# Kernel optimization log

Measured on AMD Instinct MI355X. Metric: run time of the kernel, lower is better.

## Reference

```python
import jax, jax.numpy as jnp
import numpy as np

N, L, C, H, W, HEAD = 16, 256, 512, 32, 32, 16

def setup_inputs() -> dict:
    key = jax.random.key(0)
    ks = jax.random.split(key, 8)
    s = 0.02  # weight init scale
    return {
        "feature": jax.random.normal(ks[0], (N, C, H, W), jnp.float32),
        "token": jax.random.normal(ks[1], (N, L, C), jnp.float32),
        "wq": jax.random.normal(ks[2], (C, C), jnp.float32) * s,
        "bq": jax.random.normal(ks[3], (C,), jnp.float32) * s,
        "wk": jax.random.normal(ks[4], (C, C), jnp.float32) * s,
        "bk": jax.random.normal(ks[5], (C,), jnp.float32) * s,
        "wv": jax.random.normal(ks[6], (C, C), jnp.float32) * s,
        "bv": jax.random.normal(ks[7], (C,), jnp.float32) * s,
    }

def reference(feature, token, wq, bq, wk, bk, wv, bv):
    n, c, hgt, wid = feature.shape
    h = HEAD
    d = c // h
    l = token.shape[1]
    scale = jnp.asarray(np.sqrt(c / h), feature.dtype)
    tok = token.transpose(0, 2, 1)  # (N, C, L)
    # 1x1 conv projections == per-position GEMMs
    v = (jnp.einsum('ncl,dc->ndl', tok, wv) + bv[None, :, None]).reshape(n, h, d, l)
    k = (jnp.einsum('ncl,dc->ndl', tok, wk) + bk[None, :, None]).reshape(n, h, d, l)
    q = (jnp.einsum('nchw,dc->ndhw', feature, wq) + bq[None, :, None, None])
    q = q.reshape(n, h, d, hgt * wid).transpose(0, 1, 3, 2)  # (N, h, HW, d)
    scores = jnp.einsum('nhqd,nhdl->nhql', q, k) / scale  # (N, h, HW, L)
    coef = jax.nn.softmax(scores, axis=-1)
    proj = jnp.einsum('nhdl,nhql->nhdq', v, coef)  # (N, h, d, HW)
    return feature + proj.reshape(n, c, hgt, wid)
```

## Files before the change

kernel.cpp:

```cpp
#include <hip/hip_runtime.h>
#include <hip/hip_bf16.h>

#define N_ 16
#define L_ 256
#define C_ 512
#define HW_ 1024
#define HEADS_ 16
#define DH_ 32

typedef unsigned short u16;
typedef unsigned int u32;
typedef __attribute__((ext_vector_type(8))) short short8_t;
typedef __attribute__((ext_vector_type(4))) float f32x4;

__device__ __forceinline__ u16 f2bs(float f) {
    union { float f; u32 i; } x; x.f = f;
    u32 r = x.i + 0x7fffu + ((x.i >> 16) & 1u);
    return (u16)(r >> 16);
}
__device__ __forceinline__ u32 cvt_pk_bf16(float lo, float hi) {
    u32 r;
    asm("v_cvt_pk_bf16_f32 %0, %1, %2" : "=v"(r) : "v"(lo), "v"(hi));
    return r;
}
__device__ __forceinline__ void cvt8(const float* __restrict__ src, void* dst) {
    float4 lo = *(const float4*)src;
    float4 hi = *(const float4*)(src + 4);
    union { u32 w[4]; short8_t v; } pk;
    pk.w[0] = cvt_pk_bf16(lo.x, lo.y);
    pk.w[1] = cvt_pk_bf16(lo.z, lo.w);
    pk.w[2] = cvt_pk_bf16(hi.x, hi.y);
    pk.w[3] = cvt_pk_bf16(hi.z, hi.w);
    *(short8_t*)dst = pk.v;
}
#define AS1(p) (const __attribute__((address_space(1))) void*)(p)
#define AS3(p) (__attribute__((address_space(3))) void*)(p)

__global__ __launch_bounds__(256) void prep_kv_kernel(
    const float* __restrict__ feature, const float* __restrict__ token,
    const float* __restrict__ wq, const float* __restrict__ wk,
    const float* __restrict__ wv, const float* __restrict__ bk,
    const float* __restrict__ bv,
    u16* __restrict__ Ftb, u16* __restrict__ wqb,
    u16* __restrict__ Kout, u16* __restrict__ Vt)
{
    __shared__ __align__(16) unsigned char smem[32768];
    const int t = threadIdx.x;

    if (blockIdx.x < 2048) {
        float (*LT)[67] = (float(*)[67])smem;
        const int tidx = blockIdx.x;
        const int pb = tidx & 15, cb = (tidx >> 4) & 7, n = tidx >> 7;
        const int c0 = cb * 64, pos0 = pb * 64;

        #pragma unroll
        for (int r = 0; r < 4; ++r) {
            const int c = r * 16 + (t >> 4);
            const int p = (t & 15) * 4;
            float4 v = *(const float4*)&feature[
                ((size_t)n * C_ + c0 + c) * HW_ + pos0 + p];
            LT[c][p] = v.x; LT[c][p+1] = v.y; LT[c][p+2] = v.z; LT[c][p+3] = v.w;
        }
        __syncthreads();
        #pragma unroll
        for (int rep = 0; rep < 2; ++rep) {
            const int pos = (t >> 3) + rep * 32;
            const int c = (t & 7) * 8;
            u16 tmp[8];
            #pragma unroll
            for (int j = 0; j < 8; ++j) tmp[j] = f2bs(LT[c + j][pos]);
            *(short8_t*)&Ftb[(size_t)(n * HW_ + pos0 + pos) * C_ + c0 + c] =
                *(short8_t*)tmp;
        }
    } else if (blockIdx.x < 2304) {
        const int kvid = blockIdx.x - 2048;
        const int xcd = kvid & 7, j = kvid >> 3;
        const int m0 = (xcd * 4 + (j & 3)) * 128;
        const int n0 = (j >> 2) * 64;
        const int lane = t & 63, wid = t >> 6;
        const int i16 = lane & 15, g = lane >> 4;
        const int wm = wid >> 1, wn = wid & 1;
        const int r8 = t >> 3, c8 = t & 7;
        u16* Tok = (u16*)smem;
        u16* Bk  = (u16*)(smem + 16384);
        u16* Bv  = (u16*)(smem + 24576);
        u16 (*LTo)[72] = (u16(*)[72])smem;

        f32x4 ak[4][2], av[4][2];
        #pragma unroll
        for (int mt = 0; mt < 4; ++mt)
            #pragma unroll
            for (int nt = 0; nt < 2; ++nt) {
                ak[mt][nt] = (f32x4){0.f, 0.f, 0.f, 0.f};
                av[mt][nt] = (f32x4){0.f, 0.f, 0.f, 0.f};
            }

        for (int c0 = 0; c0 < C_; c0 += 64) {
            __syncthreads();
            #pragma unroll
            for (int p = 0; p < 4; ++p) {
                const int m = p * 32 + r8;
                cvt8(&token[(size_t)(m0 + m) * C_ + c0 + c8 * 8],
                     &Tok[m * 64 + ((c8 ^ (m & 7)) << 3)]);
            }
            #pragma unroll
            for (int p = 0; p < 2; ++p) {
                const int m = p * 32 + r8;
                const int sw = m * 64 + ((c8 ^ (m & 7)) << 3);
                cvt8(&wk[(size_t)(n0 + m) * C_ + c0 + c8 * 8], &Bk[sw]);
                cvt8(&wv[(size_t)(n0 + m) * C_ + c0 + c8 * 8], &Bv[sw]);
            }
            __syncthreads();
            #pragma unroll
            for (int ks = 0; ks < 2; ++ks) {
                short8_t a[4], bbk[2], bbv[2];
                #pragma unroll
                for (int mt = 0; mt < 4; ++mt) {
                    const int m = wm * 64 + mt * 16 + i16;
                    a[mt] = *(const short8_t*)&Tok[m * 64 + ((((ks << 2) | g) ^ (m & 7)) << 3)];
                }
                #pragma unroll
                for (int nt = 0; nt < 2; ++nt) {
                    const int d = wn * 32 + nt * 16 + i16;
                    const int sw = d * 64 + ((((ks << 2) | g) ^ (d & 7)) << 3);
                    bbk[nt] = *(const short8_t*)&Bk[sw];
                    bbv[nt] = *(const short8_t*)&Bv[sw];
                }
                #pragma unroll
                for (int mt = 0; mt < 4; ++mt)
                    #pragma unroll
                    for (int nt = 0; nt < 2; ++nt) {
                        ak[mt][nt] = __builtin_amdgcn_mfma_f32_16x16x32_bf16(
                            a[mt], bbk[nt], ak[mt][nt], 0, 0, 0);
                        av[mt][nt] = __builtin_amdgcn_mfma_f32_16x16x32_bf16(
                            a[mt], bbv[nt], av[mt][nt], 0, 0, 0);
                    }
            }
        }
        const int nb = m0 >> 8, l0 = m0 & 255;
        const size_t vtbase = (size_t)nb * C_ * L_;
        #pragma unroll
        for (int nt = 0; nt < 2; ++nt) {
            const int d = n0 + wn * 32 + nt * 16 + i16;
            const float bb = bv[d];
            #pragma unroll
            for (int mt = 0; mt < 4; ++mt) {
                ushort4 w;
                w.x = f2bs(av[mt][nt][0] + bb);
                w.y = f2bs(av[mt][nt][1] + bb);
                w.z = f2bs(av[mt][nt][2] + bb);
                w.w = f2bs(av[mt][nt][3] + bb);
                const int l = l0 + wm * 64 + mt * 16 + g * 4;
                *(ushort4*)&Vt[vtbase + (size_t)d * L_ + l] = w;
            }
        }
        __syncthreads();
        #pragma unroll
        for (int nt = 0; nt < 2; ++nt) {
            const int col = wn * 32 + nt * 16 + i16;
            const float bb = bk[n0 + col];
            #pragma unroll
            for (int mt = 0; mt < 4; ++mt)
                #pragma unroll
                for (int r = 0; r < 4; ++r)
                    LTo[wm * 64 + mt * 16 + g * 4 + r][col] = f2bs(ak[mt][nt][r] + bb);
        }
        __syncthreads();
        #pragma unroll
        for (int rep = 0; rep < 4; ++rep) {
            const int m = (t >> 3) + rep * 32;
            const int cs2 = (t & 7) * 8;
            *(short8_t*)&Kout[(size_t)(m0 + m) * C_ + n0 + cs2] = *(short8_t*)&LTo[m][cs2];
        }
    } else {
        const int idx = (blockIdx.x - 2304) * 256 + t;
        float4 v = ((const float4*)wq)[idx];
        ushort4 w;
        w.x = f2bs(v.x); w.y = f2bs(v.y); w.z = f2bs(v.z); w.w = f2bs(v.w);
        ((ushort4*)wqb)[idx] = w;
    }
}

__global__ __launch_bounds__(256) void gemm_q_kernel(
    const u16* __restrict__ Ftb, const u16* __restrict__ wqb,
    const float* __restrict__ bq, u16* __restrict__ Qout)
{
    __shared__ __align__(16) unsigned char smem[65536];

    const int t = threadIdx.x;
    const int lane = t & 63, wid = t >> 6;
    const int i16 = lane & 15, g = lane >> 4;
    const int r8 = t >> 3, gr = t & 7;

    const int qid = blockIdx.x;
    const int xcd = qid & 7, loc = qid >> 3;
    const int m0 = (xcd * 16 + (loc & 15)) * 128;
    const int n0 = (loc >> 4) * 128;
    const int wm = wid >> 1, wn = wid & 1;
    u16 (*LTo)[136] = (u16(*)[136])smem;

    f32x4 aq[4][4];
    #pragma unroll
    for (int mt = 0; mt < 4; ++mt)
        #pragma unroll
        for (int nt = 0; nt < 4; ++nt)
            aq[mt][nt] = (f32x4){0.f, 0.f, 0.f, 0.f};

    #define Q_STAGE(buf, c0) { \
        _Pragma("unroll") \
        for (int p = 0; p < 4; ++p) { \
            const int row = p * 32 + r8; \
            const int gs = (gr ^ (row & 7)) << 3; \
            __builtin_amdgcn_global_load_lds( \
                AS1(Ftb + (size_t)(m0 + row) * C_ + (c0) + gs), \
                AS3(smem + (buf) * 32768 + (p * 32 + wid * 8) * 128), 16, 0, 0); \
            __builtin_amdgcn_global_load_lds( \
                AS1(wqb + (size_t)(n0 + row) * C_ + (c0) + gs), \
                AS3(smem + (buf) * 32768 + 16384 + (p * 32 + wid * 8) * 128), 16, 0, 0); } }

    Q_STAGE(0, 0);
    __syncthreads();
    #pragma unroll
    for (int cs = 0; cs < 8; ++cs) {
        const int cur = cs & 1;
        if (cs < 7) Q_STAGE(cur ^ 1, (cs + 1) * 64);
        const u16* Ft = (const u16*)(smem + cur * 32768);
        const u16* Bq = (const u16*)(smem + cur * 32768 + 16384);
        #pragma unroll
        for (int ks = 0; ks < 2; ++ks) {
            short8_t a[4], b[4];
            #pragma unroll
            for (int mt = 0; mt < 4; ++mt) {
                const int m = wm * 64 + mt * 16 + i16;
                a[mt] = *(const short8_t*)&Ft[m * 64 + ((((ks << 2) | g) ^ (m & 7)) << 3)];
            }
            #pragma unroll
            for (int nt = 0; nt < 4; ++nt) {
                const int d = wn * 64 + nt * 16 + i16;
                b[nt] = *(const short8_t*)&Bq[d * 64 + ((((ks << 2) | g) ^ (d & 7)) << 3)];
            }
            #pragma unroll
            for (int mt = 0; mt < 4; ++mt)
                #pragma unroll
                for (int nt = 0; nt < 4; ++nt)
                    aq[mt][nt] = __builtin_amdgcn_mfma_f32_16x16x32_bf16(
                        a[mt], b[nt], aq[mt][nt], 0, 0, 0);
        }
        __syncthreads();
    }
    #pragma unroll
    for (int half = 0; half < 2; ++half) {
        __syncthreads();
        if (wm == half) {
            #pragma unroll
            for (int nt = 0; nt < 4; ++nt) {
                const int col = wn * 64 + nt * 16 + i16;
                const float bb = bq[n0 + col];
                #pragma unroll
                for (int mt = 0; mt < 4; ++mt)
                    #pragma unroll
                    for (int r = 0; r < 4; ++r)
                        LTo[mt * 16 + g * 4 + r][col] = f2bs(aq[mt][nt][r] + bb);
            }
        }
        __syncthreads();
        #pragma unroll
        for (int rep = 0; rep < 4; ++rep) {
            const int row = rep * 16 + (t >> 4);
            const int col = (t & 15) * 8;
            *(short8_t*)&Qout[(size_t)(m0 + half * 64 + row) * C_ + n0 + col] =
                *(short8_t*)&LTo[row][col];
        }
    }
}

__global__ __launch_bounds__(256) void attn_kernel(
    const u16* __restrict__ Qws, const u16* __restrict__ Kws,
    const u16* __restrict__ Vws, const float* __restrict__ feature,
    float* __restrict__ out)
{
    __shared__ __align__(16) unsigned char smem[32768];

    const int t = threadIdx.x;
    const int wid = t >> 6, lane = t & 63;
    const int i16 = lane & 15, g = lane >> 4;
    const int pt = blockIdx.x, h = blockIdx.y, n = blockIdx.z;
    const int pos0 = pt * 64;
    const size_t qbase = ((size_t)n * HW_ + pos0) * C_ + h * DH_;
    const size_t kbase = ((size_t)n * L_) * C_ + h * DH_;
    const size_t vbase = (size_t)n * C_ * L_ + (size_t)h * DH_ * L_;

    const int q = wid * 16 + i16;

    short8_t bq = *(const short8_t*)&Qws[qbase + (size_t)q * C_ + g * 8];

    #pragma unroll
    for (int p = 0; p < 4; ++p) {
        const int kg = (lane & 3) ^ ((lane >> 3) & 3);
        const int kr = wid * 64 + p * 16 + (lane >> 2);
        const u16* ksrc = Kws + kbase + (size_t)kr * C_ + kg * 8;
        __builtin_amdgcn_global_load_lds(AS1(ksrc),
            AS3(smem + wid * 4096 + p * 1024), 16, 0, 0);
        const int vd = wid * 8 + p * 2 + (lane >> 5);
        const u16* vsrc = Vws + vbase + (size_t)vd * L_ + ((lane & 31) ^ (vd & 7)) * 8;
        __builtin_amdgcn_global_load_lds(AS1(vsrc),
            AS3(smem + 16384 + wid * 4096 + p * 1024), 16, 0, 0);
    }
    __syncthreads();

    const int kgr = g ^ ((i16 >> 1) & 3);
    f32x4 s[16];
    #pragma unroll
    for (int nf = 0; nf < 16; ++nf) {
        short8_t a = *(const short8_t*)(smem + (nf * 16 + i16) * 64 + kgr * 16);
        f32x4 z = {0.f, 0.f, 0.f, 0.f};
        s[nf] = __builtin_amdgcn_mfma_f32_16x16x32_bf16(a, bq, z, 0, 0, 0);
    }

    float mm[16], sm[16];
    #pragma unroll
    for (int nf = 0; nf < 16; ++nf)
        mm[nf] = fmaxf(fmaxf(s[nf][0], s[nf][1]), fmaxf(s[nf][2], s[nf][3]));
    #pragma unroll
    for (int st = 8; st >= 1; st >>= 1)
        #pragma unroll
        for (int i = 0; i < 8; ++i)
            if (i < st) mm[i] = fmaxf(mm[i], mm[i + st]);
    float m = mm[0];
    m = fmaxf(m, __shfl_xor(m, 16));
    m = fmaxf(m, __shfl_xor(m, 32));

    const float K2 = 0.25506288f;
    #pragma unroll
    for (int nf = 0; nf < 16; ++nf) {
        #pragma unroll
        for (int r = 0; r < 4; ++r) s[nf][r] = exp2f((s[nf][r] - m) * K2);
        sm[nf] = (s[nf][0] + s[nf][1]) + (s[nf][2] + s[nf][3]);
    }
    #pragma unroll
    for (int st = 8; st >= 1; st >>= 1)
        #pragma unroll
        for (int i = 0; i < 8; ++i)
            if (i < st) sm[i] += sm[i + st];
    float ssum = sm[0];
    ssum += __shfl_xor(ssum, 16);
    ssum += __shfl_xor(ssum, 32);
    const float pinv = 1.0f / ssum;

    __syncthreads();

    f32x4 o0 = {0.f, 0.f, 0.f, 0.f}, o1 = {0.f, 0.f, 0.f, 0.f};
    const int e7 = i16 & 7;

    #pragma unroll
    for (int hb = 0; hb < 2; ++hb) {
        #pragma unroll
        for (int nfp = 0; nfp < 8; ++nfp) {
            const int nf = hb * 8 + nfp;
            #pragma unroll
            for (int w = 0; w < 2; ++w) {
                u32 pw = cvt_pk_bf16(s[nf][2 * w] * pinv, s[nf][2 * w + 1] * pinv);
                const int gran = (nfp * 2 + (g >> 1)) ^ e7;
                *(u32*)(smem + q * 256 + gran * 16 + ((g & 1) * 2 + w) * 4) = pw;
            }
        }
        __syncthreads();
        #pragma unroll
        for (int ks = 0; ks < 4; ++ks) {
            short8_t pb = *(const short8_t*)(smem + q * 256 + (((ks * 4 + g) ^ e7) * 16));
            const int vg = (((hb * 4 + ks) * 4 + g) ^ e7) * 16;
            short8_t va0 = *(const short8_t*)(smem + 16384 + i16 * 512 + vg);
            short8_t va1 = *(const short8_t*)(smem + 16384 + (16 + i16) * 512 + vg);
            o0 = __builtin_amdgcn_mfma_f32_16x16x32_bf16(va0, pb, o0, 0, 0, 0);
            o1 = __builtin_amdgcn_mfma_f32_16x16x32_bf16(va1, pb, o1, 0, 0, 0);
        }
        if (hb == 0) __syncthreads();
    }

    const size_t obase = ((size_t)n * C_ + h * DH_) * HW_ + pos0 + q;
    #pragma unroll
    for (int r = 0; r < 4; ++r) {
        const size_t oa = obase + (size_t)(g * 4 + r) * HW_;
        out[oa] = feature[oa] + o0[r];
        const size_t ob = obase + (size_t)(16 + g * 4 + r) * HW_;
        out[ob] = feature[ob] + o1[r];
    }
}

extern "C" void kernel_launch(void* const* d_in, const int* in_sizes, int n_in,
                              void* d_out, int out_size, void* d_ws, size_t ws_size,
                              hipStream_t stream)
{
    const float* feature = (const float*)d_in[0];
    const float* token   = (const float*)d_in[1];
    const float* wq      = (const float*)d_in[2];
    const float* bq      = (const float*)d_in[3];
    const float* wk      = (const float*)d_in[4];
    const float* bk      = (const float*)d_in[5];
    const float* wv      = (const float*)d_in[6];
    const float* bv      = (const float*)d_in[7];
    float* out = (float*)d_out;

    u16* Qws = (u16*)d_ws;
    u16* Kws = Qws + (size_t)N_ * HW_ * C_;
    u16* Vws = Kws + (size_t)N_ * L_ * C_;

    char* ob = (char*)d_out;
    u16* Ftb = (u16*)ob;
    u16* wqb = (u16*)(ob + (21u << 20));

    prep_kv_kernel<<<dim3(2560), 256, 0, stream>>>(feature, token, wq, wk, wv,
                                                   bk, bv, Ftb, wqb, Kws, Vws);
    gemm_q_kernel<<<dim3(512), 256, 0, stream>>>(Ftb, wqb, bq, Qws);
    attn_kernel<<<dim3(16, 16, 16), 256, 0, stream>>>(Qws, Kws, Vws, feature, out);
}
```

Before: 78.95 us.

## Fuse Q projection GEMM into attention kernel, dropping separate Q GEMM

Removes the standalone Q-projection GEMM and its bf16 Q workspace round trip. Each attention block now computes its own 64x32 Q tile from bf16 feature and the matching head slice of wq, converting wq to bf16 on the fly, then rearranges the MFMA output via lane shuffles into the B-operand layout. This saves one launch and the write/read of Q. In exchange, each block re-reads feature rows across all 16 heads, and wq conversion is repeated per block.

```diff
diff --git a/kernel.cpp b/kernel.cpp
--- a/kernel.cpp
+++ b/kernel.cpp
@@ -36,44 +36,17 @@
 #define AS1(p) (const __attribute__((address_space(1))) void*)(p)
 #define AS3(p) (__attribute__((address_space(3))) void*)(p)
 
-__global__ __launch_bounds__(256) void prep_kv_kernel(
+__global__ __launch_bounds__(256) void prep_kernel(
     const float* __restrict__ feature, const float* __restrict__ token,
-    const float* __restrict__ wq, const float* __restrict__ wk,
-    const float* __restrict__ wv, const float* __restrict__ bk,
-    const float* __restrict__ bv,
-    u16* __restrict__ Ftb, u16* __restrict__ wqb,
-    u16* __restrict__ Kout, u16* __restrict__ Vt)
+    const float* __restrict__ wk, const float* __restrict__ wv,
+    const float* __restrict__ bk, const float* __restrict__ bv,
+    u16* __restrict__ Ftb, u16* __restrict__ Kout, u16* __restrict__ Vt)
 {
     __shared__ __align__(16) unsigned char smem[32768];
     const int t = threadIdx.x;
 
-    if (blockIdx.x < 2048) {
-        float (*LT)[67] = (float(*)[67])smem;
-        const int tidx = blockIdx.x;
-        const int pb = tidx & 15, cb = (tidx >> 4) & 7, n = tidx >> 7;
-        const int c0 = cb * 64, pos0 = pb * 64;
-
-        #pragma unroll
-        for (int r = 0; r < 4; ++r) {
-            const int c = r * 16 + (t >> 4);
-            const int p = (t & 15) * 4;
-            float4 v = *(const float4*)&feature[
-                ((size_t)n * C_ + c0 + c) * HW_ + pos0 + p];
-            LT[c][p] = v.x; LT[c][p+1] = v.y; LT[c][p+2] = v.z; LT[c][p+3] = v.w;
-        }
-        __syncthreads();
-        #pragma unroll
-        for (int rep = 0; rep < 2; ++rep) {
-            const int pos = (t >> 3) + rep * 32;
-            const int c = (t & 7) * 8;
-            u16 tmp[8];
-            #pragma unroll
-            for (int j = 0; j < 8; ++j) tmp[j] = f2bs(LT[c + j][pos]);
-            *(short8_t*)&Ftb[(size_t)(n * HW_ + pos0 + pos) * C_ + c0 + c] =
-                *(short8_t*)tmp;
-        }
-    } else if (blockIdx.x < 2304) {
-        const int kvid = blockIdx.x - 2048;
+    if (blockIdx.x < 256) {
+        const int kvid = blockIdx.x;
         const int xcd = kvid & 7, j = kvid >> 3;
         const int m0 = (xcd * 4 + (j & 3)) * 128;
         const int n0 = (j >> 2) * 64;
@@ -173,126 +146,116 @@
             *(short8_t*)&Kout[(size_t)(m0 + m) * C_ + n0 + cs2] = *(short8_t*)&LTo[m][cs2];
         }
     } else {
-        const int idx = (blockIdx.x - 2304) * 256 + t;
-        float4 v = ((const float4*)wq)[idx];
-        ushort4 w;
-        w.x = f2bs(v.x); w.y = f2bs(v.y); w.z = f2bs(v.z); w.w = f2bs(v.w);
-        ((ushort4*)wqb)[idx] = w;
-    }
-}
-
-__global__ __launch_bounds__(256) void gemm_q_kernel(
-    const u16* __restrict__ Ftb, const u16* __restrict__ wqb,
-    const float* __restrict__ bq, u16* __restrict__ Qout)
-{
-    __shared__ __align__(16) unsigned char smem[65536];
-
-    const int t = threadIdx.x;
-    const int lane = t & 63, wid = t >> 6;
-    const int i16 = lane & 15, g = lane >> 4;
-    const int r8 = t >> 3, gr = t & 7;
-
-    const int qid = blockIdx.x;
-    const int xcd = qid & 7, loc = qid >> 3;
-    const int m0 = (xcd * 16 + (loc & 15)) * 128;
-    const int n0 = (loc >> 4) * 128;
-    const int wm = wid >> 1, wn = wid & 1;
-    u16 (*LTo)[136] = (u16(*)[136])smem;
-
-    f32x4 aq[4][4];
-    #pragma unroll
-    for (int mt = 0; mt < 4; ++mt)
-        #pragma unroll
-        for (int nt = 0; nt < 4; ++nt)
-            aq[mt][nt] = (f32x4){0.f, 0.f, 0.f, 0.f};
-
-    #define Q_STAGE(buf, c0) { \
-        _Pragma("unroll") \
-        for (int p = 0; p < 4; ++p) { \
-            const int row = p * 32 + r8; \
-            const int gs = (gr ^ (row & 7)) << 3; \
-            __builtin_amdgcn_global_load_lds( \
-                AS1(Ftb + (size_t)(m0 + row) * C_ + (c0) + gs), \
-                AS3(smem + (buf) * 32768 + (p * 32 + wid * 8) * 128), 16, 0, 0); \
-            __builtin_amdgcn_global_load_lds( \
-                AS1(wqb + (size_t)(n0 + row) * C_ + (c0) + gs), \
-                AS3(smem + (buf) * 32768 + 16384 + (p * 32 + wid * 8) * 128), 16, 0, 0); } }
-
-    Q_STAGE(0, 0);
-    __syncthreads();
-    #pragma unroll
-    for (int cs = 0; cs < 8; ++cs) {
-        const int cur = cs & 1;
-        if (cs < 7) Q_STAGE(cur ^ 1, (cs + 1) * 64);
-        const u16* Ft = (const u16*)(smem + cur * 32768);
-        const u16* Bq = (const u16*)(smem + cur * 32768 + 16384);
-        #pragma unroll
-        for (int ks = 0; ks < 2; ++ks) {
-            short8_t a[4], b[4];
-            #pragma unroll
-            for (int mt = 0; mt < 4; ++mt) {
-                const int m = wm * 64 + mt * 16 + i16;
-                a[mt] = *(const short8_t*)&Ft[m * 64 + ((((ks << 2) | g) ^ (m & 7)) << 3)];
-            }
-            #pragma unroll
-            for (int nt = 0; nt < 4; ++nt) {
-                const int d = wn * 64 + nt * 16 + i16;
-                b[nt] = *(const short8_t*)&Bq[d * 64 + ((((ks << 2) | g) ^ (d & 7)) << 3)];
-            }
-            #pragma unroll
-            for (int mt = 0; mt < 4; ++mt)
-                #pragma unroll
-                for (int nt = 0; nt < 4; ++nt)
-                    aq[mt][nt] = __builtin_amdgcn_mfma_f32_16x16x32_bf16(
-                        a[mt], b[nt], aq[mt][nt], 0, 0, 0);
-        }
-        __syncthreads();
-    }
-    #pragma unroll
-    for (int half = 0; half < 2; ++half) {
-        __syncthreads();
-        if (wm == half) {
-            #pragma unroll
-            for (int nt = 0; nt < 4; ++nt) {
-                const int col = wn * 64 + nt * 16 + i16;
-                const float bb = bq[n0 + col];
-                #pragma unroll
-                for (int mt = 0; mt < 4; ++mt)
-                    #pragma unroll
-                    for (int r = 0; r < 4; ++r)
-                        LTo[mt * 16 + g * 4 + r][col] = f2bs(aq[mt][nt][r] + bb);
-            }
-        }
-        __syncthreads();
-        #pragma unroll
-        for (int rep = 0; rep < 4; ++rep) {
-            const int row = rep * 16 + (t >> 4);
-            const int col = (t & 15) * 8;
-            *(short8_t*)&Qout[(size_t)(m0 + half * 64 + row) * C_ + n0 + col] =
-                *(short8_t*)&LTo[row][col];
-        }
-    }
-}
-
-__global__ __launch_bounds__(256) void attn_kernel(
-    const u16* __restrict__ Qws, const u16* __restrict__ Kws,
-    const u16* __restrict__ Vws, const float* __restrict__ feature,
+        float (*LT)[67] = (float(*)[67])smem;
+        const int tidx = blockIdx.x - 256;
+        const int pb = tidx & 15, cb = (tidx >> 4) & 7, n = tidx >> 7;
+        const int c0 = cb * 64, pos0 = pb * 64;
+
+        #pragma unroll
+        for (int r = 0; r < 4; ++r) {
+            const int c = r * 16 + (t >> 4);
+            const int p = (t & 15) * 4;
+            float4 v = *(const float4*)&feature[
+                ((size_t)n * C_ + c0 + c) * HW_ + pos0 + p];
+            LT[c][p] = v.x; LT[c][p+1] = v.y; LT[c][p+2] = v.z; LT[c][p+3] = v.w;
+        }
+        __syncthreads();
+        #pragma unroll
+        for (int rep = 0; rep < 2; ++rep) {
+            const int pos = (t >> 3) + rep * 32;
+            const int c = (t & 7) * 8;
+            u16 tmp[8];
+            #pragma unroll
+            for (int j = 0; j < 8; ++j) tmp[j] = f2bs(LT[c + j][pos]);
+            *(short8_t*)&Ftb[(size_t)(n * HW_ + pos0 + pos) * C_ + c0 + c] =
+                *(short8_t*)tmp;
+        }
+    }
+}
+
+__global__ __launch_bounds__(256) void fattn_kernel(
+    const float* __restrict__ feature, const u16* __restrict__ Ftb,
+    const float* __restrict__ wq, const float* __restrict__ bqv,
+    const u16* __restrict__ Kws, const u16* __restrict__ Vws,
     float* __restrict__ out)
 {
     __shared__ __align__(16) unsigned char smem[32768];
+    const u32 QB = 12288;
 
     const int t = threadIdx.x;
     const int wid = t >> 6, lane = t & 63;
     const int i16 = lane & 15, g = lane >> 4;
-    const int pt = blockIdx.x, h = blockIdx.y, n = blockIdx.z;
+    const int h = blockIdx.x & 15;
+    const int tile = blockIdx.x >> 4;
+    const int n = tile >> 4, pt = tile & 15;
     const int pos0 = pt * 64;
-    const size_t qbase = ((size_t)n * HW_ + pos0) * C_ + h * DH_;
     const size_t kbase = ((size_t)n * L_) * C_ + h * DH_;
     const size_t vbase = (size_t)n * C_ * L_ + (size_t)h * DH_ * L_;
-
+    const size_t fbase = (size_t)(n * HW_ + pos0) * C_;
     const int q = wid * 16 + i16;
 
-    short8_t bq = *(const short8_t*)&Qws[qbase + (size_t)q * C_ + g * 8];
+    const int r8 = t >> 3, gr = t & 7;
+    f32x4 aq0 = {0.f, 0.f, 0.f, 0.f}, aq1 = {0.f, 0.f, 0.f, 0.f};
+
+    #define FQ_STAGE(buf, c0) { \
+        _Pragma("unroll") \
+        for (int p = 0; p < 2; ++p) { \
+            const int row = p * 32 + r8; \
+            __builtin_amdgcn_global_load_lds( \
+                AS1(Ftb + fbase + (size_t)row * C_ + (c0) + ((gr ^ (row & 7)) << 3)), \
+                AS3(smem + (buf) * QB + (p * 32 + wid * 8) * 128), 16, 0, 0); } \
+        { \
+            const int wrow = t >> 3; \
+            float wf[8]; \
+            const float* wsrc = wq + (size_t)(h * 32 + wrow) * C_ + (c0) + (t & 7) * 8; \
+            *(float4*)&wf[0] = *(const float4*)&wsrc[0]; \
+            *(float4*)&wf[4] = *(const float4*)&wsrc[4]; \
+            cvt8(wf, smem + (buf) * QB + 8192 + \
+                 (u32)(wrow * 128 + (((t & 7) ^ (wrow & 7)) << 4))); \
+        } }
+
+    FQ_STAGE(0, 0);
+    __syncthreads();
+    #pragma unroll
+    for (int cs = 0; cs < 8; ++cs) {
+        const int cur = cs & 1;
+        if (cs < 7) FQ_STAGE(cur ^ 1, (cs + 1) * 64);
+        #pragma unroll
+        for (int ks = 0; ks < 2; ++ks) {
+            const int browq = wid * 16 + i16;
+            short8_t b = *(const short8_t*)(smem + cur * QB +
+                (u32)(browq * 128 + ((((ks << 2) | g) ^ (browq & 7)) << 4)));
+            short8_t a0 = *(const short8_t*)(smem + cur * QB + 8192 +
+                (u32)(i16 * 128 + ((((ks << 2) | g) ^ (i16 & 7)) << 4)));
+            short8_t a1 = *(const short8_t*)(smem + cur * QB + 8192 +
+                (u32)((16 + i16) * 128 + ((((ks << 2) | g) ^ (i16 & 7)) << 4)));
+            aq0 = __builtin_amdgcn_mfma_f32_16x16x32_bf16(a0, b, aq0, 0, 0, 0);
+            aq1 = __builtin_amdgcn_mfma_f32_16x16x32_bf16(a1, b, aq1, 0, 0, 0);
+        }
+        __syncthreads();
+    }
+
+    short8_t bq;
+    {
+        float4 b0 = *(const float4*)&bqv[h * 32 + g * 4];
+        float4 b1 = *(const float4*)&bqv[h * 32 + 16 + g * 4];
+        u32 A0 = cvt_pk_bf16(aq0[0] + b0.x, aq0[1] + b0.y);
+        u32 A1 = cvt_pk_bf16(aq0[2] + b0.z, aq0[3] + b0.w);
+        u32 B0 = cvt_pk_bf16(aq1[0] + b1.x, aq1[1] + b1.y);
+        u32 B1 = cvt_pk_bf16(aq1[2] + b1.z, aq1[3] + b1.w);
+        const int srcLo = ((g & 1) * 2) * 16 + i16;
+        const int srcHi = srcLo + 16;
+        u32 XA0 = (u32)__shfl((int)A0, srcLo), XA1 = (u32)__shfl((int)A1, srcLo);
+        u32 XA2 = (u32)__shfl((int)A0, srcHi), XA3 = (u32)__shfl((int)A1, srcHi);
+        u32 XB0 = (u32)__shfl((int)B0, srcLo), XB1 = (u32)__shfl((int)B1, srcLo);
+        u32 XB2 = (u32)__shfl((int)B0, srcHi), XB3 = (u32)__shfl((int)B1, srcHi);
+        union { u32 w[4]; short8_t v; } bp;
+        bp.w[0] = g < 2 ? XA0 : XB0;
+        bp.w[1] = g < 2 ? XA1 : XB1;
+        bp.w[2] = g < 2 ? XA2 : XB2;
+        bp.w[3] = g < 2 ? XA3 : XB3;
+        bq = bp.v;
+    }
 
     #pragma unroll
     for (int p = 0; p < 4; ++p) {
@@ -401,16 +364,12 @@
     const float* bv      = (const float*)d_in[7];
     float* out = (float*)d_out;
 
-    u16* Qws = (u16*)d_ws;
-    u16* Kws = Qws + (size_t)N_ * HW_ * C_;
+    u16* Ftb = (u16*)d_ws;
+    u16* Kws = Ftb + (size_t)N_ * HW_ * C_;
     u16* Vws = Kws + (size_t)N_ * L_ * C_;
 
-    char* ob = (char*)d_out;
-    u16* Ftb = (u16*)ob;
-    u16* wqb = (u16*)(ob + (21u << 20));
-
-    prep_kv_kernel<<<dim3(2560), 256, 0, stream>>>(feature, token, wq, wk, wv,
-                                                   bk, bv, Ftb, wqb, Kws, Vws);
-    gemm_q_kernel<<<dim3(512), 256, 0, stream>>>(Ftb, wqb, bq, Qws);
-    attn_kernel<<<dim3(16, 16, 16), 256, 0, stream>>>(Qws, Kws, Vws, feature, out);
-}
+    prep_kernel<<<dim3(2304), 256, 0, stream>>>(feature, token, wk, wv,
+                                                bk, bv, Ftb, Kws, Vws);
+    fattn_kernel<<<dim3(4096), 256, 0, stream>>>(feature, Ftb, wq, bq,
+                                                 Kws, Vws, out);
+}
```

Measured after the change: 88.50 us. 1.12x slower.

## Shrink Q GEMM tile to 128x64 single-buffered and schedule KV GEMM blocks first

Applied to the files above, without the earlier changes.

The Q projection GEMM moves from 128x128 double-buffered tiles (64KB LDS, 512 blocks) to 128x64 single-buffered tiles (32KB LDS, 1024 blocks), which raises occupancy and block count at the cost of losing load/compute overlap and reloading the feature tile twice as often. The prep kernel now gives the first block indices to the longer KV projection GEMM blocks, ahead of the feature transpose blocks, so the heavier work starts first and the tail shrinks.

```diff
diff --git a/kernel.cpp b/kernel.cpp
--- a/kernel.cpp
+++ b/kernel.cpp
@@ -36,7 +36,7 @@
 #define AS1(p) (const __attribute__((address_space(1))) void*)(p)
 #define AS3(p) (__attribute__((address_space(3))) void*)(p)
 
-__global__ __launch_bounds__(256) void prep_kv_kernel(
+__global__ __launch_bounds__(256) void prep_kernel(
     const float* __restrict__ feature, const float* __restrict__ token,
     const float* __restrict__ wq, const float* __restrict__ wk,
     const float* __restrict__ wv, const float* __restrict__ bk,
@@ -47,33 +47,8 @@
     __shared__ __align__(16) unsigned char smem[32768];
     const int t = threadIdx.x;
 
-    if (blockIdx.x < 2048) {
-        float (*LT)[67] = (float(*)[67])smem;
-        const int tidx = blockIdx.x;
-        const int pb = tidx & 15, cb = (tidx >> 4) & 7, n = tidx >> 7;
-        const int c0 = cb * 64, pos0 = pb * 64;
-
-        #pragma unroll
-        for (int r = 0; r < 4; ++r) {
-            const int c = r * 16 + (t >> 4);
-            const int p = (t & 15) * 4;
-            float4 v = *(const float4*)&feature[
-                ((size_t)n * C_ + c0 + c) * HW_ + pos0 + p];
-            LT[c][p] = v.x; LT[c][p+1] = v.y; LT[c][p+2] = v.z; LT[c][p+3] = v.w;
-        }
-        __syncthreads();
-        #pragma unroll
-        for (int rep = 0; rep < 2; ++rep) {
-            const int pos = (t >> 3) + rep * 32;
-            const int c = (t & 7) * 8;
-            u16 tmp[8];
-            #pragma unroll
-            for (int j = 0; j < 8; ++j) tmp[j] = f2bs(LT[c + j][pos]);
-            *(short8_t*)&Ftb[(size_t)(n * HW_ + pos0 + pos) * C_ + c0 + c] =
-                *(short8_t*)tmp;
-        }
-    } else if (blockIdx.x < 2304) {
-        const int kvid = blockIdx.x - 2048;
+    if (blockIdx.x < 256) {
+        const int kvid = blockIdx.x;
         const int xcd = kvid & 7, j = kvid >> 3;
         const int m0 = (xcd * 4 + (j & 3)) * 128;
         const int n0 = (j >> 2) * 64;
@@ -172,6 +147,31 @@
             const int cs2 = (t & 7) * 8;
             *(short8_t*)&Kout[(size_t)(m0 + m) * C_ + n0 + cs2] = *(short8_t*)&LTo[m][cs2];
         }
+    } else if (blockIdx.x < 2304) {
+        float (*LT)[67] = (float(*)[67])smem;
+        const int tidx = blockIdx.x - 256;
+        const int pb = tidx & 15, cb = (tidx >> 4) & 7, n = tidx >> 7;
+        const int c0 = cb * 64, pos0 = pb * 64;
+
+        #pragma unroll
+        for (int r = 0; r < 4; ++r) {
+            const int c = r * 16 + (t >> 4);
+            const int p = (t & 15) * 4;
+            float4 v = *(const float4*)&feature[
+                ((size_t)n * C_ + c0 + c) * HW_ + pos0 + p];
+            LT[c][p] = v.x; LT[c][p+1] = v.y; LT[c][p+2] = v.z; LT[c][p+3] = v.w;
+        }
+        __syncthreads();
+        #pragma unroll
+        for (int rep = 0; rep < 2; ++rep) {
+            const int pos = (t >> 3) + rep * 32;
+            const int c = (t & 7) * 8;
+            u16 tmp[8];
+            #pragma unroll
+            for (int j = 0; j < 8; ++j) tmp[j] = f2bs(LT[c + j][pos]);
+            *(short8_t*)&Ftb[(size_t)(n * HW_ + pos0 + pos) * C_ + c0 + c] =
+                *(short8_t*)tmp;
+        }
     } else {
         const int idx = (blockIdx.x - 2304) * 256 + t;
         float4 v = ((const float4*)wq)[idx];
@@ -185,92 +185,84 @@
     const u16* __restrict__ Ftb, const u16* __restrict__ wqb,
     const float* __restrict__ bq, u16* __restrict__ Qout)
 {
-    __shared__ __align__(16) unsigned char smem[65536];
+    __shared__ __align__(16) unsigned char smem[32768];
 
     const int t = threadIdx.x;
     const int lane = t & 63, wid = t >> 6;
     const int i16 = lane & 15, g = lane >> 4;
+    const int wm = wid >> 1, wn = wid & 1;
     const int r8 = t >> 3, gr = t & 7;
 
     const int qid = blockIdx.x;
-    const int xcd = qid & 7, loc = qid >> 3;
-    const int m0 = (xcd * 16 + (loc & 15)) * 128;
-    const int n0 = (loc >> 4) * 128;
-    const int wm = wid >> 1, wn = wid & 1;
-    u16 (*LTo)[136] = (u16(*)[136])smem;
-
-    f32x4 aq[4][4];
+    const int xcd = qid & 7, j = qid >> 3;
+    const int m0 = (xcd * 16 + (j & 15)) * 128;
+    const int n0 = (j >> 4) * 64;
+    u16* Ft = (u16*)smem;
+    u16* Bq = (u16*)(smem + 16384);
+    u16 (*LTo)[72] = (u16(*)[72])smem;
+
+    f32x4 aq[4][2];
     #pragma unroll
     for (int mt = 0; mt < 4; ++mt)
         #pragma unroll
-        for (int nt = 0; nt < 4; ++nt)
+        for (int nt = 0; nt < 2; ++nt)
             aq[mt][nt] = (f32x4){0.f, 0.f, 0.f, 0.f};
 
-    #define Q_STAGE(buf, c0) { \
-        _Pragma("unroll") \
-        for (int p = 0; p < 4; ++p) { \
-            const int row = p * 32 + r8; \
-            const int gs = (gr ^ (row & 7)) << 3; \
-            __builtin_amdgcn_global_load_lds( \
-                AS1(Ftb + (size_t)(m0 + row) * C_ + (c0) + gs), \
-                AS3(smem + (buf) * 32768 + (p * 32 + wid * 8) * 128), 16, 0, 0); \
-            __builtin_amdgcn_global_load_lds( \
-                AS1(wqb + (size_t)(n0 + row) * C_ + (c0) + gs), \
-                AS3(smem + (buf) * 32768 + 16384 + (p * 32 + wid * 8) * 128), 16, 0, 0); } }
-
-    Q_STAGE(0, 0);
-    __syncthreads();
-    #pragma unroll
-    for (int cs = 0; cs < 8; ++cs) {
-        const int cur = cs & 1;
-        if (cs < 7) Q_STAGE(cur ^ 1, (cs + 1) * 64);
-        const u16* Ft = (const u16*)(smem + cur * 32768);
-        const u16* Bq = (const u16*)(smem + cur * 32768 + 16384);
+    for (int c0 = 0; c0 < C_; c0 += 64) {
+        __syncthreads();
+        #pragma unroll
+        for (int p = 0; p < 4; ++p) {
+            const int row = p * 32 + r8;
+            __builtin_amdgcn_global_load_lds(
+                AS1(Ftb + (size_t)(m0 + row) * C_ + c0 + ((gr ^ (row & 7)) << 3)),
+                AS3(smem + (p * 32 + wid * 8) * 128), 16, 0, 0);
+        }
+        #pragma unroll
+        for (int p = 0; p < 2; ++p) {
+            const int row = p * 32 + r8;
+            __builtin_amdgcn_global_load_lds(
+                AS1(wqb + (size_t)(n0 + row) * C_ + c0 + ((gr ^ (row & 7)) << 3)),
+                AS3(smem + 16384 + (p * 32 + wid * 8) * 128), 16, 0, 0);
+        }
+        __syncthreads();
         #pragma unroll
         for (int ks = 0; ks < 2; ++ks) {
-            short8_t a[4], b[4];
+            short8_t a[4], b[2];
             #pragma unroll
             for (int mt = 0; mt < 4; ++mt) {
                 const int m = wm * 64 + mt * 16 + i16;
                 a[mt] = *(const short8_t*)&Ft[m * 64 + ((((ks << 2) | g) ^ (m & 7)) << 3)];
             }
             #pragma unroll
-            for (int nt = 0; nt < 4; ++nt) {
-                const int d = wn * 64 + nt * 16 + i16;
+            for (int nt = 0; nt < 2; ++nt) {
+                const int d = wn * 32 + nt * 16 + i16;
                 b[nt] = *(const short8_t*)&Bq[d * 64 + ((((ks << 2) | g) ^ (d & 7)) << 3)];
             }
             #pragma unroll
             for (int mt = 0; mt < 4; ++mt)
                 #pragma unroll
-                for (int nt = 0; nt < 4; ++nt)
+                for (int nt = 0; nt < 2; ++nt)
                     aq[mt][nt] = __builtin_amdgcn_mfma_f32_16x16x32_bf16(
                         a[mt], b[nt], aq[mt][nt], 0, 0, 0);
         }
-        __syncthreads();
-    }
-    #pragma unroll
-    for (int half = 0; half < 2; ++half) {
-        __syncthreads();
-        if (wm == half) {
-            #pragma unroll
-            for (int nt = 0; nt < 4; ++nt) {
-                const int col = wn * 64 + nt * 16 + i16;
-                const float bb = bq[n0 + col];
-                #pragma unroll
-                for (int mt = 0; mt < 4; ++mt)
-                    #pragma unroll
-                    for (int r = 0; r < 4; ++r)
-                        LTo[mt * 16 + g * 4 + r][col] = f2bs(aq[mt][nt][r] + bb);
-            }
-        }
-        __syncthreads();
-        #pragma unroll
-        for (int rep = 0; rep < 4; ++rep) {
-            const int row = rep * 16 + (t >> 4);
-            const int col = (t & 15) * 8;
-            *(short8_t*)&Qout[(size_t)(m0 + half * 64 + row) * C_ + n0 + col] =
-                *(short8_t*)&LTo[row][col];
-        }
+    }
+    __syncthreads();
+    #pragma unroll
+    for (int nt = 0; nt < 2; ++nt) {
+        const int col = wn * 32 + nt * 16 + i16;
+        const float bb = bq[n0 + col];
+        #pragma unroll
+        for (int mt = 0; mt < 4; ++mt)
+            #pragma unroll
+            for (int r = 0; r < 4; ++r)
+                LTo[wm * 64 + mt * 16 + g * 4 + r][col] = f2bs(aq[mt][nt][r] + bb);
+    }
+    __syncthreads();
+    #pragma unroll
+    for (int rep = 0; rep < 4; ++rep) {
+        const int m = (t >> 3) + rep * 32;
+        const int cs = (t & 7) * 8;
+        *(short8_t*)&Qout[(size_t)(m0 + m) * C_ + n0 + cs] = *(short8_t*)&LTo[m][cs];
     }
 }
 
@@ -409,8 +401,8 @@
     u16* Ftb = (u16*)ob;
     u16* wqb = (u16*)(ob + (21u << 20));
 
-    prep_kv_kernel<<<dim3(2560), 256, 0, stream>>>(feature, token, wq, wk, wv,
-                                                   bk, bv, Ftb, wqb, Kws, Vws);
-    gemm_q_kernel<<<dim3(512), 256, 0, stream>>>(Ftb, wqb, bq, Qws);
+    prep_kernel<<<dim3(2560), 256, 0, stream>>>(feature, token, wq, wk, wv,
+                                                bk, bv, Ftb, wqb, Kws, Vws);
+    gemm_q_kernel<<<dim3(1024), 256, 0, stream>>>(Ftb, wqb, bq, Qws);
     attn_kernel<<<dim3(16, 16, 16), 256, 0, stream>>>(Qws, Kws, Vws, feature, out);
 }
```

New measurement: 73.08 us. -7.4%, faster.
